# Kernel tuning notes

Hardware: AMD Instinct MI355X
Metric: run time of the kernel (lower is better)

The kernel has to match this reference:

```python
import jax, jax.numpy as jnp
import numpy as np

EMBED = 1024
HEADS = 16
DH = EMBED // HEADS
B, S = 2, 2048


def setup_inputs() -> dict:
    key = jax.random.key(0)
    ks = jax.random.split(key, 12)
    inp = {
        "k": jax.random.normal(ks[0], (B, S, EMBED), jnp.float32),
        "q": jax.random.normal(ks[1], (B, S, EMBED), jnp.float32),
        "v": jax.random.normal(ks[2], (B, S, EMBED), jnp.float32),
        "mask": jax.random.randint(ks[3], (B, 1, S, S), 0, 2, jnp.int32),
        # per-head projections (shared across heads, as in the torch module)
        "Wk": jax.random.normal(ks[4], (DH, DH), jnp.float32) / np.sqrt(DH),
        "bk": jnp.zeros((DH,), jnp.float32),
        "Wq": jax.random.normal(ks[5], (DH, DH), jnp.float32) / np.sqrt(DH),
        "bq": jnp.zeros((DH,), jnp.float32),
        "Wv": jax.random.normal(ks[6], (DH, DH), jnp.float32) / np.sqrt(DH),
        "bv": jnp.zeros((DH,), jnp.float32),
        "Wo": jax.random.normal(ks[7], (EMBED, EMBED), jnp.float32) / np.sqrt(EMBED),
        "bo": jnp.zeros((EMBED,), jnp.float32),
    }
    return inp


def reference(k, q, v, mask, Wk, bk, Wq, bq, Wv, bv, Wo, bo):
    b, s, _ = k.shape
    sq = q.shape[1]
    # [B,S,H,dh]
    kh = k.reshape(b, s, HEADS, DH)
    qh = q.reshape(b, sq, HEADS, DH)
    vh = v.reshape(b, s, HEADS, DH)
    # per-head linear (weight shared across heads): x @ W.T + b
    kh = kh @ Wk.T + bk
    qh = qh @ Wq.T + bq
    vh = vh @ Wv.T + bv
    # scores [B,H,Sq,Sk]
    product = jnp.einsum("bqhd,bkhd->bhqk", qh, kh)
    # masked_fill BEFORE scaling, as in the original
    product = jnp.where(mask == 0, jnp.float32(-1e20), product)
    product = product / np.sqrt(DH)
    scores = jax.nn.softmax(product, axis=-1)
    ctx = jnp.einsum("bhqk,bkhd->bqhd", scores, vh).reshape(b, sq, EMBED)
    return ctx @ Wo.T + bo
```

## Files before the change

### kernel.cpp

```cpp
#include <hip/hip_runtime.h>
#include <hip/hip_bf16.h>
#include <math.h>

#define EMBED 1024
#define HEADS 16
#define DH    64
#define BATCH 2
#define SEQ   2048

typedef __attribute__((ext_vector_type(8))) short bf16x8;
typedef __attribute__((ext_vector_type(4))) short bf16x4;
typedef __attribute__((ext_vector_type(4))) float f32x4;
typedef unsigned long long u64;

static __device__ __forceinline__ unsigned short f2bf(float x) {
    unsigned u = __builtin_bit_cast(unsigned, x);
    return (unsigned short)((u + 0x7fffu + ((u >> 16) & 1u)) >> 16);
}

__global__ __launch_bounds__(256) void proj_mfma(
    const float* __restrict__ q, const float* __restrict__ k, const float* __restrict__ v,
    const float* __restrict__ Wq, const float* __restrict__ bq,
    const float* __restrict__ Wk, const float* __restrict__ bk,
    const float* __restrict__ Wv, const float* __restrict__ bv,
    unsigned short* __restrict__ qh, unsigned short* __restrict__ kh,
    unsigned short* __restrict__ vh)
{
    const int blk = blockIdx.x;
    const int which = blockIdx.y;
    const float* x; const float* W; const float* bias; unsigned short* out;
    if (which == 0)      { x = q; W = Wq; bias = bq; out = qh; }
    else if (which == 1) { x = k; W = Wk; bias = bk; out = kh; }
    else                 { x = v; W = Wv; bias = bv; out = vh; }

    __shared__ unsigned short Xs[64 * 72];
    __shared__ unsigned short Ws[64 * 72];

    const int t  = threadIdx.x;
    const int sr = t >> 2, sp = t & 3;

    {
        const float* xsrc = x + ((size_t)blk * 64 + sr) * 64 + sp * 16;
        unsigned short o[16];
#pragma unroll
        for (int u4 = 0; u4 < 4; ++u4) {
            float4 a = ((const float4*)xsrc)[u4];
            o[u4*4+0] = f2bf(a.x); o[u4*4+1] = f2bf(a.y);
            o[u4*4+2] = f2bf(a.z); o[u4*4+3] = f2bf(a.w);
        }
        *(uint4*)&Xs[sr * 72 + sp * 16]     = *(uint4*)&o[0];
        *(uint4*)&Xs[sr * 72 + sp * 16 + 8] = *(uint4*)&o[8];
        const float* wsrc = W + (size_t)sr * 64 + sp * 16;
        unsigned short wo[16];
#pragma unroll
        for (int u4 = 0; u4 < 4; ++u4) {
            float4 a = ((const float4*)wsrc)[u4];
            wo[u4*4+0] = f2bf(a.x); wo[u4*4+1] = f2bf(a.y);
            wo[u4*4+2] = f2bf(a.z); wo[u4*4+3] = f2bf(a.w);
        }
        *(uint4*)&Ws[sr * 72 + sp * 16]     = *(uint4*)&wo[0];
        *(uint4*)&Ws[sr * 72 + sp * 16 + 8] = *(uint4*)&wo[8];
    }
    __syncthreads();

    const int w    = t >> 6;
    const int lane = t & 63;
    const int l15  = lane & 15;
    const int quad = lane >> 4;

    bf16x8 af0 = *(const bf16x8*)&Xs[(w * 16 + l15) * 72 + quad * 8];
    bf16x8 af1 = *(const bf16x8*)&Xs[(w * 16 + l15) * 72 + 32 + quad * 8];

    f32x4 acc[4];
#pragma unroll
    for (int nt = 0; nt < 4; ++nt) {
        bf16x8 bf0 = *(const bf16x8*)&Ws[(nt * 16 + l15) * 72 + quad * 8];
        bf16x8 bf1 = *(const bf16x8*)&Ws[(nt * 16 + l15) * 72 + 32 + quad * 8];
        f32x4 a = {0, 0, 0, 0};
        a = __builtin_amdgcn_mfma_f32_16x16x32_bf16(af0, bf0, a, 0, 0, 0);
        a = __builtin_amdgcn_mfma_f32_16x16x32_bf16(af1, bf1, a, 0, 0, 0);
        acc[nt] = a;
    }

    const int bsidx = blk * 4 + w;
    const int b = bsidx >> 11, s = bsidx & 2047;
#pragma unroll
    for (int nt = 0; nt < 4; ++nt) {
        const int d = nt * 16 + l15;
        const float bb = bias[d];
#pragma unroll
        for (int r = 0; r < 4; ++r) {
            const int h = quad * 4 + r;
            out[(((size_t)b * HEADS + h) * SEQ + s) * DH + d] = f2bf(acc[nt][r] + bb);
        }
    }
}

__global__ __launch_bounds__(256) void vtrans_kernel(
    const unsigned short* __restrict__ vh, unsigned short* __restrict__ vt)
{
    const int st = blockIdx.x;
    const int bh = blockIdx.y;
    __shared__ unsigned short Tt[64 * 72];

    const int t = threadIdx.x;
    const int r = t >> 2, p = t & 3;

    const unsigned short* src = vh + ((size_t)bh * SEQ + st * 64 + r) * DH + p * 16;
    *(uint4*)&Tt[r * 72 + p * 16]     = *(const uint4*)src;
    *(uint4*)&Tt[r * 72 + p * 16 + 8] = *(const uint4*)(src + 8);
    __syncthreads();

    union { unsigned short u[16]; uint4 v[2]; } o;
#pragma unroll
    for (int u = 0; u < 16; ++u) o.u[u] = Tt[(p * 16 + u) * 72 + r];
    unsigned short* dst = vt + ((size_t)bh * DH + r) * SEQ + st * 64 + p * 16;
    *(uint4*)dst       = o.v[0];
    *(uint4*)(dst + 8) = o.v[1];
}

__global__ __launch_bounds__(256) void maskpack_kernel(
    const int* __restrict__ mask, u64* __restrict__ bits)
{
    const int idx = blockIdx.x * 256 + threadIdx.x;
    const int4* src = (const int4*)(mask + (size_t)idx * 64);
    u64 w = 0;
#pragma unroll
    for (int u = 0; u < 16; ++u) {
        int4 m = src[u];
        u64 nib = (m.x != 0 ? 1ull : 0) | (m.y != 0 ? 2ull : 0) |
                  (m.z != 0 ? 4ull : 0) | (m.w != 0 ? 8ull : 0);
        w |= nib << (u * 4);
    }
    bits[idx] = w;
}

__global__ __launch_bounds__(256) void wcvt_kernel(
    const float* __restrict__ Wo, unsigned short* __restrict__ Wob)
{
    const int i = (blockIdx.x * 256 + threadIdx.x) * 8;
    float4 a = ((const float4*)(Wo + i))[0];
    float4 b = ((const float4*)(Wo + i))[1];
    unsigned short o[8] = {f2bf(a.x), f2bf(a.y), f2bf(a.z), f2bf(a.w),
                           f2bf(b.x), f2bf(b.y), f2bf(b.z), f2bf(b.w)};
    *(uint4*)(Wob + i) = *(uint4*)o;
}

__global__ __launch_bounds__(512, 4) void attn_kernel(
    const unsigned short* __restrict__ qh, const unsigned short* __restrict__ kh,
    const unsigned short* __restrict__ vt, const u64* __restrict__ mbits,
    unsigned short* __restrict__ ctx)
{
    const int bid = blockIdx.x;
    const int bh  = bid & 31;
    const int q0  = (bid >> 5) * 128;
    const int b   = bh >> 4;

    __shared__ uint4 smem4[2304];
    unsigned short* KtH = ((unsigned short*)smem4) + (threadIdx.x >> 8) * 9216;
    unsigned short* VtH = KtH + 4608;

    const int t    = threadIdx.x;
    const int half = t >> 8;
    const int w    = (t >> 6) & 3;
    const int lane = t & 63;
    const int l15  = lane & 15;
    const int quad = lane >> 4;
    const int t2   = t & 255;
    const int sr   = t2 >> 2, sp = t2 & 3;

    bf16x8 qf[2][2];
#pragma unroll
    for (int g = 0; g < 2; ++g) {
        const unsigned short* qb =
            qh + ((size_t)bh * SEQ + q0 + w * 32 + g * 16 + l15) * DH + quad * 8;
        qf[g][0] = *(const bf16x8*)qb;
        qf[g][1] = *(const bf16x8*)(qb + 32);
    }

    f32x4 O[2][4];
#pragma unroll
    for (int g = 0; g < 2; ++g)
#pragma unroll
        for (int dt = 0; dt < 4; ++dt) O[g][dt] = f32x4{0, 0, 0, 0};
    float lsum[2] = {0.f, 0.f};

    const unsigned short* kbase = kh + (size_t)bh * SEQ * DH + (size_t)half * 1024 * DH;
    const unsigned short* vbase = vt + (size_t)bh * DH * SEQ + half * 1024;
    const u64* mrow0 = mbits + ((size_t)b * SEQ + q0 + w * 32 + l15) * (SEQ / 64) + half * 16;
    const u64* mrow1 = mrow0 + 16 * (SEQ / 64);

    uint4 pk0, pk1, pv0, pv1;
    u64 pm0, pm1;
    {
        const unsigned short* ks = kbase + (size_t)sr * DH + sp * 16;
        pk0 = *(const uint4*)ks; pk1 = *(const uint4*)(ks + 8);
        const unsigned short* vs = vbase + (size_t)sr * SEQ + sp * 16;
        pv0 = *(const uint4*)vs; pv1 = *(const uint4*)(vs + 8);
        pm0 = mrow0[0]; pm1 = mrow1[0];
    }

    for (int kt = 0; kt < 16; ++kt) {
        __syncthreads();
        *(uint4*)&KtH[sr * 72 + sp * 16]     = pk0;
        *(uint4*)&KtH[sr * 72 + sp * 16 + 8] = pk1;
        *(uint4*)&VtH[sr * 72 + sp * 16]     = pv0;
        *(uint4*)&VtH[sr * 72 + sp * 16 + 8] = pv1;
        const u64 mb0 = pm0, mb1 = pm1;
        if (kt < 15) {
            const unsigned short* ks = kbase + (size_t)((kt + 1) * 64 + sr) * DH + sp * 16;
            pk0 = *(const uint4*)ks; pk1 = *(const uint4*)(ks + 8);
            const unsigned short* vs = vbase + (size_t)sr * SEQ + (kt + 1) * 64 + sp * 16;
            pv0 = *(const uint4*)vs; pv1 = *(const uint4*)(vs + 8);
            pm0 = mrow0[kt + 1]; pm1 = mrow1[kt + 1];
        }
        __syncthreads();

        bf16x4 p[2][4];
#pragma unroll
        for (int st = 0; st < 4; ++st) {
            bf16x8 kf0 = *(const bf16x8*)&KtH[(st * 16 + l15) * 72 + quad * 8];
            bf16x8 kf1 = *(const bf16x8*)&KtH[(st * 16 + l15) * 72 + 32 + quad * 8];
#pragma unroll
            for (int g = 0; g < 2; ++g) {
                f32x4 sa = {0, 0, 0, 0};
                sa = __builtin_amdgcn_mfma_f32_16x16x32_bf16(kf0, qf[g][0], sa, 0, 0, 0);
                sa = __builtin_amdgcn_mfma_f32_16x16x32_bf16(kf1, qf[g][1], sa, 0, 0, 0);
                const unsigned nib = (unsigned)((g ? mb1 : mb0) >> (st * 16 + quad * 4)) & 0xFu;
                float p0 = (nib & 1u) ? __expf(sa[0] * 0.125f) : 0.f;
                float p1 = (nib & 2u) ? __expf(sa[1] * 0.125f) : 0.f;
                float p2 = (nib & 4u) ? __expf(sa[2] * 0.125f) : 0.f;
                float p3 = (nib & 8u) ? __expf(sa[3] * 0.125f) : 0.f;
                lsum[g] += (p0 + p1) + (p2 + p3);
                union { __hip_bfloat162 h2[2]; bf16x4 v; } pu;
                pu.h2[0] = __float22bfloat162_rn(make_float2(p0, p1));
                pu.h2[1] = __float22bfloat162_rn(make_float2(p2, p3));
                p[g][st] = pu.v;
            }
        }

#pragma unroll
        for (int dt = 0; dt < 4; ++dt) {
#pragma unroll
            for (int st = 0; st < 4; ++st) {
                bf16x4 vb = *(const bf16x4*)&VtH[(dt * 16 + l15) * 72 + st * 16 + quad * 4];
                O[0][dt] = __builtin_amdgcn_mfma_f32_16x16x16bf16_1k(p[0][st], vb, O[0][dt], 0, 0, 0);
                O[1][dt] = __builtin_amdgcn_mfma_f32_16x16x16bf16_1k(p[1][st], vb, O[1][dt], 0, 0, 0);
            }
        }
    }

    float lr[2];
#pragma unroll
    for (int g = 0; g < 2; ++g) {
        lr[g] = lsum[g];
        lr[g] += __shfl_xor(lr[g], 16);
        lr[g] += __shfl_xor(lr[g], 32);
    }

    float* Obuf = (float*)smem4;
    float* Ls   = ((float*)smem4) + 128 * 66;

    __syncthreads();
    if (half == 0) {
#pragma unroll
        for (int g = 0; g < 2; ++g)
#pragma unroll
            for (int dt = 0; dt < 4; ++dt)
#pragma unroll
                for (int r = 0; r < 4; ++r)
                    Obuf[(w * 32 + g * 16 + quad * 4 + r) * 66 + dt * 16 + l15] = O[g][dt][r];
        if (quad == 0) {
            Ls[w * 32 + l15]      = lr[0];
            Ls[w * 32 + 16 + l15] = lr[1];
        }
    }
    __syncthreads();
    if (half == 1) {
#pragma unroll
        for (int g = 0; g < 2; ++g) {
            const float ltot = lr[g] + Ls[w * 32 + g * 16 + l15];
            const float invl = 1.0f / ltot;
            float invr[4];
#pragma unroll
            for (int r = 0; r < 4; ++r) invr[r] = __shfl(invl, quad * 4 + r);
#pragma unroll
            for (int r = 0; r < 4; ++r) {
                const int row = w * 32 + g * 16 + quad * 4 + r;
                unsigned short* dst = ctx + ((size_t)bh * SEQ + q0 + row) * DH + l15;
#pragma unroll
                for (int dt = 0; dt < 4; ++dt) {
                    const float val = O[g][dt][r] + Obuf[row * 66 + dt * 16 + l15];
                    dst[dt * 16] = f2bf(val * invr[r]);
                }
            }
        }
    }
}

__global__ __launch_bounds__(256) void outproj_mfma(
    const unsigned short* __restrict__ ctx, const unsigned short* __restrict__ Wob,
    const float* __restrict__ bo, float* __restrict__ out)
{
    const int n0 = blockIdx.x * 64;
    const int m0 = blockIdx.y * 64;
    const int b  = m0 / SEQ;
    const int s0 = m0 % SEQ;

    __shared__ unsigned short At[64 * 72];
    __shared__ unsigned short Wt[64 * 72];

    const int t    = threadIdx.x;
    const int w    = t >> 6;
    const int lane = t & 63;
    const int l15  = lane & 15;
    const int quad = lane >> 4;
    const int sr = t >> 2, sp = t & 3;

    f32x4 acc[4] = {f32x4{0,0,0,0}, f32x4{0,0,0,0}, f32x4{0,0,0,0}, f32x4{0,0,0,0}};

    for (int kt = 0; kt < HEADS; ++kt) {
        __syncthreads();
        {
            const unsigned short* as =
                ctx + (((size_t)b * HEADS + kt) * SEQ + s0 + sr) * DH + sp * 16;
            *(uint4*)&At[sr * 72 + sp * 16]     = *(const uint4*)as;
            *(uint4*)&At[sr * 72 + sp * 16 + 8] = *(const uint4*)(as + 8);
            const unsigned short* wsrc =
                Wob + (size_t)(n0 + sr) * EMBED + kt * 64 + sp * 16;
            *(uint4*)&Wt[sr * 72 + sp * 16]     = *(const uint4*)wsrc;
            *(uint4*)&Wt[sr * 72 + sp * 16 + 8] = *(const uint4*)(wsrc + 8);
        }
        __syncthreads();

        bf16x8 bf0 = *(const bf16x8*)&Wt[(w * 16 + l15) * 72 + quad * 8];
        bf16x8 bf1 = *(const bf16x8*)&Wt[(w * 16 + l15) * 72 + 32 + quad * 8];
#pragma unroll
        for (int mt = 0; mt < 4; ++mt) {
            bf16x8 af0 = *(const bf16x8*)&At[(mt * 16 + l15) * 72 + quad * 8];
            bf16x8 af1 = *(const bf16x8*)&At[(mt * 16 + l15) * 72 + 32 + quad * 8];
            acc[mt] = __builtin_amdgcn_mfma_f32_16x16x32_bf16(af0, bf0, acc[mt], 0, 0, 0);
            acc[mt] = __builtin_amdgcn_mfma_f32_16x16x32_bf16(af1, bf1, acc[mt], 0, 0, 0);
        }
    }

    const float bv = bo[n0 + w * 16 + l15];
#pragma unroll
    for (int mt = 0; mt < 4; ++mt) {
#pragma unroll
        for (int r = 0; r < 4; ++r) {
            out[(size_t)(m0 + mt * 16 + quad * 4 + r) * EMBED + n0 + w * 16 + l15] =
                acc[mt][r] + bv;
        }
    }
}

extern "C" void kernel_launch(void* const* d_in, const int* in_sizes, int n_in,
                              void* d_out, int out_size, void* d_ws, size_t ws_size,
                              hipStream_t stream) {
    const float* k    = (const float*)d_in[0];
    const float* q    = (const float*)d_in[1];
    const float* v    = (const float*)d_in[2];
    const int*   mask = (const int*)  d_in[3];
    const float* Wk   = (const float*)d_in[4];
    const float* bk   = (const float*)d_in[5];
    const float* Wq   = (const float*)d_in[6];
    const float* bq   = (const float*)d_in[7];
    const float* Wv   = (const float*)d_in[8];
    const float* bv   = (const float*)d_in[9];
    const float* Wo   = (const float*)d_in[10];
    const float* bo   = (const float*)d_in[11];
    float* out = (float*)d_out;

    const size_t TEN = (size_t)BATCH * HEADS * SEQ * DH;
    unsigned short* qh_bf = (unsigned short*)d_ws;
    unsigned short* kh_bf = qh_bf + TEN;
    unsigned short* vh_bf = kh_bf + TEN;
    unsigned short* vt_bf = vh_bf + TEN;
    unsigned short* ctxb  = vt_bf + TEN;
    unsigned short* Wob   = ctxb + TEN;
    u64*            mbits = (u64*)(Wob + EMBED * EMBED);

    proj_mfma<<<dim3(BATCH * SEQ * HEADS / 64, 3), 256, 0, stream>>>(
        q, k, v, Wq, bq, Wk, bk, Wv, bv, qh_bf, kh_bf, vh_bf);
    vtrans_kernel<<<dim3(SEQ / 64, BATCH * HEADS), 256, 0, stream>>>(vh_bf, vt_bf);
    maskpack_kernel<<<dim3((BATCH * SEQ * (SEQ / 64)) / 256), 256, 0, stream>>>(mask, mbits);
    wcvt_kernel<<<dim3(EMBED * EMBED / (256 * 8)), 256, 0, stream>>>(Wo, Wob);
    attn_kernel<<<dim3((SEQ / 128) * BATCH * HEADS), 512, 0, stream>>>(
        qh_bf, kh_bf, vt_bf, mbits, ctxb);
    outproj_mfma<<<dim3(EMBED / 64, BATCH * SEQ / 64), 256, 0, stream>>>(
        ctxb, Wob, bo, out);
}
```

Baseline: 255.0 us.

## Fuse prep kernels, fold softmax scale into Q, shrink attention blocks

Merges the V-transpose, mask-packing and Wo conversion kernels into one prep kernel to cut launch count. Pre-multiplies Q by log2(e)/sqrt(dh) so the softmax uses exp2f without a per-element multiply. Computes the row sums with an MFMA against a ones vector instead of scalar adds and cross-lane shuffles. Attention blocks shrink from 512 to 256 threads covering 64 query rows each, which doubles the grid and the number of K/V tile loads. Each thread now stages 64 bytes per tile instead of 32.

```diff
diff --git a/kernel.cpp b/kernel.cpp
--- a/kernel.cpp
+++ b/kernel.cpp
@@ -13,9 +13,16 @@
 typedef __attribute__((ext_vector_type(4))) float f32x4;
 typedef unsigned long long u64;
 
+#define QSCALE 0.1803368801111244f
+
 static __device__ __forceinline__ unsigned short f2bf(float x) {
     unsigned u = __builtin_bit_cast(unsigned, x);
     return (unsigned short)((u + 0x7fffu + ((u >> 16) & 1u)) >> 16);
+}
+static __device__ __forceinline__ unsigned pk2bf(float a, float b) {
+    union { __hip_bfloat162 h2; unsigned u; } c;
+    c.h2 = __float22bfloat162_rn(make_float2(a, b));
+    return c.u;
 }
 
 __global__ __launch_bounds__(256) void proj_mfma(
@@ -32,6 +39,7 @@
     if (which == 0)      { x = q; W = Wq; bias = bq; out = qh; }
     else if (which == 1) { x = k; W = Wk; bias = bk; out = kh; }
     else                 { x = v; W = Wv; bias = bv; out = vh; }
+    const float oscale = (which == 0) ? QSCALE : 1.0f;
 
     __shared__ unsigned short Xs[64 * 72];
     __shared__ unsigned short Ws[64 * 72];
@@ -41,25 +49,24 @@
 
     {
         const float* xsrc = x + ((size_t)blk * 64 + sr) * 64 + sp * 16;
-        unsigned short o[16];
+        unsigned o32[8];
 #pragma unroll
         for (int u4 = 0; u4 < 4; ++u4) {
             float4 a = ((const float4*)xsrc)[u4];
-            o[u4*4+0] = f2bf(a.x); o[u4*4+1] = f2bf(a.y);
-            o[u4*4+2] = f2bf(a.z); o[u4*4+3] = f2bf(a.w);
-        }
-        *(uint4*)&Xs[sr * 72 + sp * 16]     = *(uint4*)&o[0];
-        *(uint4*)&Xs[sr * 72 + sp * 16 + 8] = *(uint4*)&o[8];
+            o32[u4 * 2 + 0] = pk2bf(a.x, a.y);
+            o32[u4 * 2 + 1] = pk2bf(a.z, a.w);
+        }
+        *(uint4*)&Xs[sr * 72 + sp * 16]     = *(uint4*)&o32[0];
+        *(uint4*)&Xs[sr * 72 + sp * 16 + 8] = *(uint4*)&o32[4];
         const float* wsrc = W + (size_t)sr * 64 + sp * 16;
-        unsigned short wo[16];
 #pragma unroll
         for (int u4 = 0; u4 < 4; ++u4) {
             float4 a = ((const float4*)wsrc)[u4];
-            wo[u4*4+0] = f2bf(a.x); wo[u4*4+1] = f2bf(a.y);
-            wo[u4*4+2] = f2bf(a.z); wo[u4*4+3] = f2bf(a.w);
-        }
-        *(uint4*)&Ws[sr * 72 + sp * 16]     = *(uint4*)&wo[0];
-        *(uint4*)&Ws[sr * 72 + sp * 16 + 8] = *(uint4*)&wo[8];
+            o32[u4 * 2 + 0] = pk2bf(a.x, a.y);
+            o32[u4 * 2 + 1] = pk2bf(a.z, a.w);
+        }
+        *(uint4*)&Ws[sr * 72 + sp * 16]     = *(uint4*)&o32[0];
+        *(uint4*)&Ws[sr * 72 + sp * 16 + 8] = *(uint4*)&o32[4];
     }
     __syncthreads();
 
@@ -91,89 +98,90 @@
 #pragma unroll
         for (int r = 0; r < 4; ++r) {
             const int h = quad * 4 + r;
-            out[(((size_t)b * HEADS + h) * SEQ + s) * DH + d] = f2bf(acc[nt][r] + bb);
-        }
-    }
-}
-
-__global__ __launch_bounds__(256) void vtrans_kernel(
-    const unsigned short* __restrict__ vh, unsigned short* __restrict__ vt)
-{
-    const int st = blockIdx.x;
-    const int bh = blockIdx.y;
-    __shared__ unsigned short Tt[64 * 72];
-
-    const int t = threadIdx.x;
-    const int r = t >> 2, p = t & 3;
-
-    const unsigned short* src = vh + ((size_t)bh * SEQ + st * 64 + r) * DH + p * 16;
-    *(uint4*)&Tt[r * 72 + p * 16]     = *(const uint4*)src;
-    *(uint4*)&Tt[r * 72 + p * 16 + 8] = *(const uint4*)(src + 8);
-    __syncthreads();
-
-    union { unsigned short u[16]; uint4 v[2]; } o;
-#pragma unroll
-    for (int u = 0; u < 16; ++u) o.u[u] = Tt[(p * 16 + u) * 72 + r];
-    unsigned short* dst = vt + ((size_t)bh * DH + r) * SEQ + st * 64 + p * 16;
-    *(uint4*)dst       = o.v[0];
-    *(uint4*)(dst + 8) = o.v[1];
-}
-
-__global__ __launch_bounds__(256) void maskpack_kernel(
-    const int* __restrict__ mask, u64* __restrict__ bits)
-{
-    const int idx = blockIdx.x * 256 + threadIdx.x;
-    const int4* src = (const int4*)(mask + (size_t)idx * 64);
-    u64 w = 0;
-#pragma unroll
-    for (int u = 0; u < 16; ++u) {
-        int4 m = src[u];
-        u64 nib = (m.x != 0 ? 1ull : 0) | (m.y != 0 ? 2ull : 0) |
-                  (m.z != 0 ? 4ull : 0) | (m.w != 0 ? 8ull : 0);
-        w |= nib << (u * 4);
-    }
-    bits[idx] = w;
-}
-
-__global__ __launch_bounds__(256) void wcvt_kernel(
+            out[(((size_t)b * HEADS + h) * SEQ + s) * DH + d] =
+                f2bf((acc[nt][r] + bb) * oscale);
+        }
+    }
+}
+
+__global__ __launch_bounds__(256) void prep_kernel(
+    const unsigned short* __restrict__ vh, unsigned short* __restrict__ vt,
+    const int* __restrict__ mask, u64* __restrict__ bits,
     const float* __restrict__ Wo, unsigned short* __restrict__ Wob)
 {
-    const int i = (blockIdx.x * 256 + threadIdx.x) * 8;
-    float4 a = ((const float4*)(Wo + i))[0];
-    float4 b = ((const float4*)(Wo + i))[1];
-    unsigned short o[8] = {f2bf(a.x), f2bf(a.y), f2bf(a.z), f2bf(a.w),
-                           f2bf(b.x), f2bf(b.y), f2bf(b.z), f2bf(b.w)};
-    *(uint4*)(Wob + i) = *(uint4*)o;
-}
-
-__global__ __launch_bounds__(512, 4) void attn_kernel(
+    __shared__ unsigned short Tt[64 * 72];
+    const int bid = blockIdx.x;
+    const int t   = threadIdx.x;
+
+    if (bid < 1024) {
+        const int st = bid & 31;
+        const int bh = bid >> 5;
+        const int r = t >> 2, p = t & 3;
+        const unsigned short* src = vh + ((size_t)bh * SEQ + st * 64 + r) * DH + p * 16;
+        *(uint4*)&Tt[r * 72 + p * 16]     = *(const uint4*)src;
+        *(uint4*)&Tt[r * 72 + p * 16 + 8] = *(const uint4*)(src + 8);
+        __syncthreads();
+        union { unsigned short u[16]; uint4 v[2]; } o;
+#pragma unroll
+        for (int u = 0; u < 16; ++u) o.u[u] = Tt[(p * 16 + u) * 72 + r];
+        unsigned short* dst = vt + ((size_t)bh * DH + r) * SEQ + st * 64 + p * 16;
+        *(uint4*)dst       = o.v[0];
+        *(uint4*)(dst + 8) = o.v[1];
+    } else if (bid < 1536) {
+        const int idx = (bid - 1024) * 256 + t;
+        const int4* src = (const int4*)(mask + (size_t)idx * 64);
+        u64 w = 0;
+#pragma unroll
+        for (int u = 0; u < 16; ++u) {
+            int4 m = src[u];
+            u64 nib = (m.x != 0 ? 1ull : 0) | (m.y != 0 ? 2ull : 0) |
+                      (m.z != 0 ? 4ull : 0) | (m.w != 0 ? 8ull : 0);
+            w |= nib << (u * 4);
+        }
+        bits[idx] = w;
+    } else {
+        const int i = ((bid - 1536) * 256 + t) * 8;
+        float4 a = ((const float4*)(Wo + i))[0];
+        float4 b = ((const float4*)(Wo + i))[1];
+        unsigned o32[4] = {pk2bf(a.x, a.y), pk2bf(a.z, a.w),
+                           pk2bf(b.x, b.y), pk2bf(b.z, b.w)};
+        *(uint4*)(Wob + i) = *(uint4*)o32;
+    }
+}
+
+__global__ __launch_bounds__(256, 4) void attn_kernel(
     const unsigned short* __restrict__ qh, const unsigned short* __restrict__ kh,
     const unsigned short* __restrict__ vt, const u64* __restrict__ mbits,
     unsigned short* __restrict__ ctx)
 {
     const int bid = blockIdx.x;
     const int bh  = bid & 31;
-    const int q0  = (bid >> 5) * 128;
+    const int q0  = (bid >> 5) * 64;
     const int b   = bh >> 4;
 
     __shared__ uint4 smem4[2304];
-    unsigned short* KtH = ((unsigned short*)smem4) + (threadIdx.x >> 8) * 9216;
-    unsigned short* VtH = KtH + 4608;
+    unsigned short* smem = (unsigned short*)smem4;
 
     const int t    = threadIdx.x;
-    const int half = t >> 8;
-    const int w    = (t >> 6) & 3;
+    const int hh   = t >> 7;
+    const int w2   = (t >> 6) & 1;
     const int lane = t & 63;
     const int l15  = lane & 15;
     const int quad = lane >> 4;
-    const int t2   = t & 255;
-    const int sr   = t2 >> 2, sp = t2 & 3;
+
+    unsigned short* KtH = smem + hh * 9216;
+    unsigned short* VtH = KtH + 4608;
+
+    const int t3 = t & 127;
+    const int sr = t3 >> 1, sp = t3 & 1;
+    unsigned short* Kdst = smem + hh * 9216 + sr * 72 + sp * 32;
+    unsigned short* Vdst = Kdst + 4608;
 
     bf16x8 qf[2][2];
 #pragma unroll
     for (int g = 0; g < 2; ++g) {
         const unsigned short* qb =
-            qh + ((size_t)bh * SEQ + q0 + w * 32 + g * 16 + l15) * DH + quad * 8;
+            qh + ((size_t)bh * SEQ + q0 + w2 * 32 + g * 16 + l15) * DH + quad * 8;
         qf[g][0] = *(const bf16x8*)qb;
         qf[g][1] = *(const bf16x8*)(qb + 32);
     }
@@ -183,35 +191,43 @@
     for (int g = 0; g < 2; ++g)
 #pragma unroll
         for (int dt = 0; dt < 4; ++dt) O[g][dt] = f32x4{0, 0, 0, 0};
-    float lsum[2] = {0.f, 0.f};
-
-    const unsigned short* kbase = kh + (size_t)bh * SEQ * DH + (size_t)half * 1024 * DH;
-    const unsigned short* vbase = vt + (size_t)bh * DH * SEQ + half * 1024;
-    const u64* mrow0 = mbits + ((size_t)b * SEQ + q0 + w * 32 + l15) * (SEQ / 64) + half * 16;
+    f32x4 Osum[2] = {f32x4{0, 0, 0, 0}, f32x4{0, 0, 0, 0}};
+    const bf16x4 ones = {(short)0x3F80, (short)0x3F80, (short)0x3F80, (short)0x3F80};
+
+    const unsigned short* kbase = kh + (size_t)bh * SEQ * DH + (size_t)hh * 1024 * DH;
+    const unsigned short* vbase = vt + (size_t)bh * DH * SEQ + hh * 1024;
+    const u64* mrow0 = mbits + ((size_t)b * SEQ + q0 + w2 * 32 + l15) * (SEQ / 64) + hh * 16;
     const u64* mrow1 = mrow0 + 16 * (SEQ / 64);
 
-    uint4 pk0, pk1, pv0, pv1;
+    uint4 pk[4], pv[4];
     u64 pm0, pm1;
     {
-        const unsigned short* ks = kbase + (size_t)sr * DH + sp * 16;
-        pk0 = *(const uint4*)ks; pk1 = *(const uint4*)(ks + 8);
-        const unsigned short* vs = vbase + (size_t)sr * SEQ + sp * 16;
-        pv0 = *(const uint4*)vs; pv1 = *(const uint4*)(vs + 8);
+        const unsigned short* ks = kbase + (size_t)sr * DH + sp * 32;
+        const unsigned short* vs = vbase + (size_t)sr * SEQ + sp * 32;
+#pragma unroll
+        for (int u = 0; u < 4; ++u) {
+            pk[u] = *(const uint4*)(ks + u * 8);
+            pv[u] = *(const uint4*)(vs + u * 8);
+        }
         pm0 = mrow0[0]; pm1 = mrow1[0];
     }
 
     for (int kt = 0; kt < 16; ++kt) {
         __syncthreads();
-        *(uint4*)&KtH[sr * 72 + sp * 16]     = pk0;
-        *(uint4*)&KtH[sr * 72 + sp * 16 + 8] = pk1;
-        *(uint4*)&VtH[sr * 72 + sp * 16]     = pv0;
-        *(uint4*)&VtH[sr * 72 + sp * 16 + 8] = pv1;
+#pragma unroll
+        for (int u = 0; u < 4; ++u) {
+            *(uint4*)(Kdst + u * 8) = pk[u];
+            *(uint4*)(Vdst + u * 8) = pv[u];
+        }
         const u64 mb0 = pm0, mb1 = pm1;
         if (kt < 15) {
-            const unsigned short* ks = kbase + (size_t)((kt + 1) * 64 + sr) * DH + sp * 16;
-            pk0 = *(const uint4*)ks; pk1 = *(const uint4*)(ks + 8);
-            const unsigned short* vs = vbase + (size_t)sr * SEQ + (kt + 1) * 64 + sp * 16;
-            pv0 = *(const uint4*)vs; pv1 = *(const uint4*)(vs + 8);
+            const unsigned short* ks = kbase + (size_t)((kt + 1) * 64 + sr) * DH + sp * 32;
+            const unsigned short* vs = vbase + (size_t)sr * SEQ + (kt + 1) * 64 + sp * 32;
+#pragma unroll
+            for (int u = 0; u < 4; ++u) {
+                pk[u] = *(const uint4*)(ks + u * 8);
+                pv[u] = *(const uint4*)(vs + u * 8);
+            }
             pm0 = mrow0[kt + 1]; pm1 = mrow1[kt + 1];
         }
         __syncthreads();
@@ -227,15 +243,15 @@
                 sa = __builtin_amdgcn_mfma_f32_16x16x32_bf16(kf0, qf[g][0], sa, 0, 0, 0);
                 sa = __builtin_amdgcn_mfma_f32_16x16x32_bf16(kf1, qf[g][1], sa, 0, 0, 0);
                 const unsigned nib = (unsigned)((g ? mb1 : mb0) >> (st * 16 + quad * 4)) & 0xFu;
-                float p0 = (nib & 1u) ? __expf(sa[0] * 0.125f) : 0.f;
-                float p1 = (nib & 2u) ? __expf(sa[1] * 0.125f) : 0.f;
-                float p2 = (nib & 4u) ? __expf(sa[2] * 0.125f) : 0.f;
-                float p3 = (nib & 8u) ? __expf(sa[3] * 0.125f) : 0.f;
-                lsum[g] += (p0 + p1) + (p2 + p3);
-                union { __hip_bfloat162 h2[2]; bf16x4 v; } pu;
-                pu.h2[0] = __float22bfloat162_rn(make_float2(p0, p1));
-                pu.h2[1] = __float22bfloat162_rn(make_float2(p2, p3));
+                float p0 = (nib & 1u) ? exp2f(sa[0]) : 0.f;
+                float p1 = (nib & 2u) ? exp2f(sa[1]) : 0.f;
+                float p2 = (nib & 4u) ? exp2f(sa[2]) : 0.f;
+                float p3 = (nib & 8u) ? exp2f(sa[3]) : 0.f;
+                union { unsigned u2[2]; bf16x4 v; } pu;
+                pu.u2[0] = pk2bf(p0, p1);
+                pu.u2[1] = pk2bf(p2, p3);
                 p[g][st] = pu.v;
+                Osum[g] = __builtin_amdgcn_mfma_f32_16x16x16bf16_1k(p[g][st], ones, Osum[g], 0, 0, 0);
             }
         }
 
@@ -250,43 +266,38 @@
         }
     }
 
-    float lr[2];
-#pragma unroll
-    for (int g = 0; g < 2; ++g) {
-        lr[g] = lsum[g];
-        lr[g] += __shfl_xor(lr[g], 16);
-        lr[g] += __shfl_xor(lr[g], 32);
-    }
-
     float* Obuf = (float*)smem4;
-    float* Ls   = ((float*)smem4) + 128 * 66;
+    float* Ls   = ((float*)smem4) + 64 * 66;
 
     __syncthreads();
-    if (half == 0) {
-#pragma unroll
-        for (int g = 0; g < 2; ++g)
+    if (hh == 0) {
+#pragma unroll
+        for (int g = 0; g < 2; ++g) {
 #pragma unroll
             for (int dt = 0; dt < 4; ++dt)
 #pragma unroll
                 for (int r = 0; r < 4; ++r)
-                    Obuf[(w * 32 + g * 16 + quad * 4 + r) * 66 + dt * 16 + l15] = O[g][dt][r];
-        if (quad == 0) {
-            Ls[w * 32 + l15]      = lr[0];
-            Ls[w * 32 + 16 + l15] = lr[1];
+                    Obuf[(w2 * 32 + g * 16 + quad * 4 + r) * 66 + dt * 16 + l15] = O[g][dt][r];
+            if (l15 == 0) {
+#pragma unroll
+                for (int r = 0; r < 4; ++r)
+                    Ls[w2 * 32 + g * 16 + quad * 4 + r] = Osum[g][r];
+            }
         }
     }
     __syncthreads();
-    if (half == 1) {
+    if (hh == 1) {
 #pragma unroll
         for (int g = 0; g < 2; ++g) {
-            const float ltot = lr[g] + Ls[w * 32 + g * 16 + l15];
-            const float invl = 1.0f / ltot;
             float invr[4];
 #pragma unroll
-            for (int r = 0; r < 4; ++r) invr[r] = __shfl(invl, quad * 4 + r);
-#pragma unroll
             for (int r = 0; r < 4; ++r) {
-                const int row = w * 32 + g * 16 + quad * 4 + r;
+                const int row = w2 * 32 + g * 16 + quad * 4 + r;
+                invr[r] = 1.0f / (Osum[g][r] + Ls[row]);
+            }
+#pragma unroll
+            for (int r = 0; r < 4; ++r) {
+                const int row = w2 * 32 + g * 16 + quad * 4 + r;
                 unsigned short* dst = ctx + ((size_t)bh * SEQ + q0 + row) * DH + l15;
 #pragma unroll
                 for (int dt = 0; dt < 4; ++dt) {
@@ -383,10 +394,9 @@
 
     proj_mfma<<<dim3(BATCH * SEQ * HEADS / 64, 3), 256, 0, stream>>>(
         q, k, v, Wq, bq, Wk, bk, Wv, bv, qh_bf, kh_bf, vh_bf);
-    vtrans_kernel<<<dim3(SEQ / 64, BATCH * HEADS), 256, 0, stream>>>(vh_bf, vt_bf);
-    maskpack_kernel<<<dim3((BATCH * SEQ * (SEQ / 64)) / 256), 256, 0, stream>>>(mask, mbits);
-    wcvt_kernel<<<dim3(EMBED * EMBED / (256 * 8)), 256, 0, stream>>>(Wo, Wob);
-    attn_kernel<<<dim3((SEQ / 128) * BATCH * HEADS), 512, 0, stream>>>(
+    prep_kernel<<<dim3(2048), 256, 0, stream>>>(
+        vh_bf, vt_bf, mask, mbits, Wo, Wob);
+    attn_kernel<<<dim3((SEQ / 64) * BATCH * HEADS), 256, 0, stream>>>(
         qh_bf, kh_bf, vt_bf, mbits, ctxb);
     outproj_mfma<<<dim3(EMBED / 64, BATCH * SEQ / 64), 256, 0, stream>>>(
         ctxb, Wob, bo, out);
```

New measurement: 379.5 us. +48.9%, slower.
